# Kernel tuning notes

Measured on AMD Instinct MI355X. Metric: run time of the kernel, lower is better.

The kernel has to match this reference:

```python
import jax, jax.numpy as jnp
import numpy as np

NB_CLASSES = 10  # matches init_kwargs nb_classes


def setup_inputs() -> dict:
    key = jax.random.key(0)
    k1, k2 = jax.random.split(key)
    N, D = 500_000, 64
    h = jax.random.normal(k1, (N, D), dtype=jnp.float32)
    yhat = jax.random.randint(k2, (N,), 0, NB_CLASSES, dtype=jnp.int32)
    return {"h": h, "yhat": yhat}


def reference(h, yhat):
    # Original torch loop: for each class k, gather h_k = h[yhat==k],
    # M_k = mean_i(h_i h_i^T) * 0.5 + I, loss += 0.5 * logdet(M_k).
    # mean of outer products == (masked h)^T @ h / count_k, so we avoid
    # the ragged gather and any [N, D, D] intermediate entirely.
    N, D = h.shape
    eye = jnp.eye(D, dtype=h.dtype)

    def class_term(k):
        mask = (yhat == k).astype(h.dtype)            # [N]
        count = jnp.sum(mask)                         # B_k
        gram = jnp.einsum('nd,ne->de', mask[:, None] * h, h)  # sum_i h_i h_i^T
        M = gram * (0.5 / count) + eye                # [D, D], SPD
        _, logabsdet = jnp.linalg.slogdet(M)
        return 0.5 * logabsdet

    # NB_CLASSES is a small fixed constant -> Python loop is fine & keeps
    # peak memory at one extra [N, D] buffer.
    return jnp.sum(jnp.stack([class_term(k) for k in range(NB_CLASSES)]))
```

## Files before the change

### kernel.cpp

```cpp
#include <hip/hip_runtime.h>
#include <hip/hip_bf16.h>

typedef __attribute__((ext_vector_type(8))) short  short8;
typedef __attribute__((ext_vector_type(4))) float  f32x4;

#define NCLS 10
#define TILE 128
#define TPB  1024
#define NQ   10
#define PPB  (NCLS * NQ * 256)
#define CH   8

#define AS1 __attribute__((address_space(1)))
#define AS3 __attribute__((address_space(3)))

static __device__ inline unsigned short f2bf(float x) {
    unsigned u = __builtin_bit_cast(unsigned, x);
    unsigned r = (u + 0x7FFFu + ((u >> 16) & 1u)) >> 16;
    return (unsigned short)r;
}

static __device__ __forceinline__ void issue_tile(
        const float* __restrict__ h, const int* __restrict__ yhat,
        float* fsb, int* yb, long t, int wid, int lane) {
    const size_t tb = (size_t)t * (TILE * 64);
#pragma unroll
    for (int i = 0; i < 2; ++i) {
        const int C   = (wid * 2 + i) * 64 + lane;
        const int row = C >> 4;
        const int qc  = C & 15;
        const float* gp = h + tb + row * 64 + ((qc ^ (row & 3)) << 2);
        __builtin_amdgcn_global_load_lds((const AS1 float*)gp,
                                         (AS3 float*)(fsb + (wid * 2 + i) * 256),
                                         16, 0, 0);
    }
    if (wid == 0 && lane < 32) {
        const int* gy = yhat + (size_t)t * TILE + lane * 4;
        __builtin_amdgcn_global_load_lds((const AS1 int*)gy, (AS3 int*)yb, 16, 0, 0);
    }
}

template<int NS>
static __device__ __forceinline__ void compute_range(
        const char* hsb, const char* mkb,
        int cls, int ks0, int hi, int col, f32x4 (&acc)[NQ]) {
    const int cb = col << 8;
    const int c7 = col & 7;
#pragma unroll
    for (int s = 0; s < NS; ++s) {
        const int ks = ks0 + s;
        const short8 m = *reinterpret_cast<const short8*>(mkb + cls * 256 + ks * 64 + hi * 16);
        const int x = ((ks * 4 + hi) ^ c7) << 4;
        short8 am[4];
#pragma unroll
        for (int nb = 0; nb < 4; ++nb) {
            short8 r = *reinterpret_cast<const short8*>(hsb + nb * 4096 + cb + x);
            am[nb] = r & m;
        }
        acc[0] = __builtin_amdgcn_mfma_f32_16x16x32_bf16(am[0], am[0], acc[0], 0, 0, 0);
        acc[1] = __builtin_amdgcn_mfma_f32_16x16x32_bf16(am[0], am[1], acc[1], 0, 0, 0);
        acc[2] = __builtin_amdgcn_mfma_f32_16x16x32_bf16(am[0], am[2], acc[2], 0, 0, 0);
        acc[3] = __builtin_amdgcn_mfma_f32_16x16x32_bf16(am[0], am[3], acc[3], 0, 0, 0);
        acc[4] = __builtin_amdgcn_mfma_f32_16x16x32_bf16(am[1], am[1], acc[4], 0, 0, 0);
        acc[5] = __builtin_amdgcn_mfma_f32_16x16x32_bf16(am[1], am[2], acc[5], 0, 0, 0);
        acc[6] = __builtin_amdgcn_mfma_f32_16x16x32_bf16(am[1], am[3], acc[6], 0, 0, 0);
        acc[7] = __builtin_amdgcn_mfma_f32_16x16x32_bf16(am[2], am[2], acc[7], 0, 0, 0);
        acc[8] = __builtin_amdgcn_mfma_f32_16x16x32_bf16(am[2], am[3], acc[8], 0, 0, 0);
        acc[9] = __builtin_amdgcn_mfma_f32_16x16x32_bf16(am[3], am[3], acc[9], 0, 0, 0);
    }
}

__global__ __launch_bounds__(TPB, 4) void HL_gram(
        const float* __restrict__ h, const int* __restrict__ yhat,
        float* __restrict__ partials, int* __restrict__ cntp,
        int N, int ntiles, int G) {
    __shared__ __align__(16) float          fs[2][TILE * 64];
    __shared__ __align__(16) unsigned short hs[2][64 * TILE];
    __shared__ __align__(16) unsigned short mk[2][NCLS * TILE];
    __shared__ __align__(16) int            ylds[2][TILE];
    __shared__ int cntlds[16];

    const int tid  = threadIdx.x;
    const int wid  = tid >> 6;
    const int lane = tid & 63;
    const int hi   = lane >> 4;
    const int col  = lane & 15;
    const int r2   = tid >> 4;
    const int q16  = tid & 15;

    if (tid < 16) cntlds[tid] = 0;

    int cls, ks0, ns;
    if      (wid < 6)  { cls = wid;      ks0 = 0; ns = 2; }
    else if (wid < 10) { cls = wid;      ks0 = 0; ns = 4; }
    else               { cls = wid - 10; ks0 = 2; ns = 2; }

    f32x4 acc[NQ];
#pragma unroll
    for (int q = 0; q < NQ; ++q) acc[q] = (f32x4){0.f, 0.f, 0.f, 0.f};

    const int  bid     = blockIdx.x;
    const int  K       = (ntiles - bid + G - 1) / G;
    const bool partial = (N % TILE) != 0;

    if (!(partial && bid == ntiles - 1))
        issue_tile(h, yhat, &fs[0][0], &ylds[0][0], bid, wid, lane);

    int cur = 0;
    for (int k = 0; k < K; ++k) {
        const long t    = bid + (long)k * G;
        const bool tail = partial && (t == (long)(ntiles - 1));

        __syncthreads();

        f32x4 v[2];
#pragma unroll
        for (int j = 0; j < 2; ++j) {
            const int row = r2 * 2 + j;
            if (!tail) {
                v[j] = *reinterpret_cast<const f32x4*>(
                    (const char*)&fs[cur][0] + ((row * 256 + (q16 << 4)) ^ ((row & 3) << 4)));
            } else {
                const long g = t * TILE + row;
                if (g < N) v[j] = *reinterpret_cast<const f32x4*>(h + (size_t)g * 64 + (q16 << 2));
                else       v[j] = (f32x4){0.f, 0.f, 0.f, 0.f};
            }
        }
#pragma unroll
        for (int q = 0; q < 4; ++q) {
            const int d = q16 * 4 + q;
            unsigned pk = (unsigned)f2bf(v[0][q]) | ((unsigned)f2bf(v[1][q]) << 16);
            *reinterpret_cast<unsigned*>(
                (char*)&hs[cur][0] + ((d * 256 + r2 * 4) ^ ((d & 7) << 4))) = pk;
        }
        if (tid < TILE) {
            int y;
            if (!tail) y = ylds[cur][tid];
            else { const long g = t * TILE + tid; y = (g < N) ? yhat[g] : -1; }
#pragma unroll
            for (int c = 0; c < NCLS; ++c) {
                mk[cur][c * TILE + tid] = (y == c) ? (unsigned short)0xFFFFu : (unsigned short)0u;
                unsigned long long b = __ballot(y == c);
                if (lane == 0) atomicAdd(&cntlds[c], __popcll(b));
            }
        }

        __syncthreads();

        if (k + 1 < K) {
            const long tn = bid + (long)(k + 1) * G;
            if (!(partial && tn == (long)(ntiles - 1)))
                issue_tile(h, yhat, &fs[cur ^ 1][0], &ylds[cur ^ 1][0], tn, wid, lane);
        }

        if (ns == 4) compute_range<4>((const char*)&hs[cur][0], (const char*)&mk[cur][0],
                                      cls, 0,   hi, col, acc);
        else         compute_range<2>((const char*)&hs[cur][0], (const char*)&mk[cur][0],
                                      cls, ks0, hi, col, acc);
        cur ^= 1;
    }

    float* xch = (float*)&fs[0][0];
#pragma unroll
    for (int qq = 0; qq < NQ; qq += 2) {
        __syncthreads();
        if (wid >= 10) {
            float* dst = xch + (wid - 10) * 512;
            *reinterpret_cast<f32x4*>(dst + (lane << 2))       = acc[qq];
            *reinterpret_cast<f32x4*>(dst + 256 + (lane << 2)) = acc[qq + 1];
        }
        __syncthreads();
        if (wid < 6) {
            const float* src = xch + wid * 512;
            acc[qq]     += *reinterpret_cast<const f32x4*>(src + (lane << 2));
            acc[qq + 1] += *reinterpret_cast<const f32x4*>(src + 256 + (lane << 2));
        }
    }

    if (wid < NCLS) {
        float* pb = partials + (size_t)bid * PPB + (size_t)wid * (NQ * 256);
#pragma unroll
        for (int q = 0; q < NQ; ++q)
            *reinterpret_cast<f32x4*>(pb + q * 256 + (lane << 2)) = acc[q];
    }
    if (tid < NCLS) cntp[bid * 16 + tid] = cntlds[tid];
}

__global__ void HL_reduce(const float* __restrict__ partials, float* __restrict__ rpart,
                          float* __restrict__ out, int G, int CS) {
    const int idx = blockIdx.x * blockDim.x + threadIdx.x;
    if (blockIdx.x == 0 && threadIdx.x == 0) out[0] = 0.f;
    if (idx >= CH * NCLS * NQ * 64) return;
    const int ch = idx / (NCLS * NQ * 64);
    const int r  = idx % (NCLS * NQ * 64);
    const int cq = r >> 6;
    const int l  = r & 63;

    int b0 = ch * CS;
    int b1 = b0 + CS; if (b1 > G) b1 = G;

    f32x4 s = (f32x4){0.f, 0.f, 0.f, 0.f};
    const float* p = partials + (size_t)cq * 256 + (l << 2);
    for (int b = b0; b < b1; ++b)
        s += *reinterpret_cast<const f32x4*>(p + (size_t)b * PPB);

    *reinterpret_cast<f32x4*>(rpart + ((size_t)ch * (NCLS * NQ) + cq) * 256 + (l << 2)) = s;
}

__global__ __launch_bounds__(64, 1) void HL_chol(
        const float* __restrict__ rpart, const int* __restrict__ cntp,
        float* __restrict__ out, int G) {
    __shared__ float M[64][68];
    __shared__ float lcol[64];
    const int cls = blockIdx.x;
    const int i   = threadIdx.x;

    int c = 0;
    for (int b = i; b < G; b += 64) c += cntp[b * 16 + cls];
#pragma unroll
    for (int off = 32; off > 0; off >>= 1) c += __shfl_xor(c, off);
    const float inv = 0.5f / (float)c;

    const int QMB[NQ] = {0,0,0,0,1,1,1,2,2,3};
    const int QNB[NQ] = {0,1,2,3,1,2,3,2,3,3};
    const float* rp = rpart + (size_t)cls * (NQ * 256);
#pragma unroll
    for (int q = 0; q < NQ; ++q) {
        f32x4 s = (f32x4){0.f, 0.f, 0.f, 0.f};
#pragma unroll
        for (int ch = 0; ch < CH; ++ch)
            s += *reinterpret_cast<const f32x4*>(rp + (size_t)ch * (NCLS * NQ * 256) + q * 256 + (i << 2));
        const int row0 = QMB[q] * 16 + ((i >> 4) << 2);
        const int colo = QNB[q] * 16 + (i & 15);
#pragma unroll
        for (int rr = 0; rr < 4; ++rr) {
            M[row0 + rr][colo] = s[rr];
            M[colo][row0 + rr] = s[rr];
        }
    }
    __syncthreads();

    float row[64];
#pragma unroll
    for (int c2 = 0; c2 < 64; ++c2)
        row[c2] = M[i][c2] * inv + (c2 == i ? 1.0f : 0.0f);

#pragma unroll
    for (int j = 0; j < 64; ++j) {
        const float piv = __shfl(row[j], j);
        const float li  = row[j] * rsqrtf(piv);
        lcol[i] = li;
        __syncthreads();
#pragma unroll
        for (int c2 = j + 1; c2 < 64; ++c2)
            row[c2] -= li * lcol[c2];
        __syncthreads();
    }

    float slog = 0.f;
#pragma unroll
    for (int j = 0; j < 64; ++j)
        if (i == j) slog = __logf(row[j]);
    slog += __shfl_down(slog, 32); slog += __shfl_down(slog, 16);
    slog += __shfl_down(slog, 8);  slog += __shfl_down(slog, 4);
    slog += __shfl_down(slog, 2);  slog += __shfl_down(slog, 1);
    if (i == 0) atomicAdd(out, 0.5f * slog);
}

extern "C" void kernel_launch(void* const* d_in, const int* in_sizes, int n_in,
                              void* d_out, int out_size, void* d_ws, size_t ws_size,
                              hipStream_t stream) {
    const float* h    = (const float*)d_in[0];
    const int*   yhat = (const int*)d_in[1];
    const int    N    = in_sizes[1];
    float* out = (float*)d_out;

    const size_t rpart_sz = (size_t)CH * NCLS * NQ * 256 * sizeof(float);
    const size_t cntp_off = rpart_sz;

    const int ntiles = (N + TILE - 1) / TILE;
    int G = 256;
    {
        const size_t perG = 64 + (size_t)PPB * sizeof(float);
        if (ws_size > rpart_sz) {
            size_t maxG = (ws_size - rpart_sz) / perG;
            if ((size_t)G > maxG) G = (int)maxG;
        } else G = 1;
        if (G < 1) G = 1;
    }
    if (G > ntiles) G = ntiles;

    const size_t partials_off = cntp_off + (size_t)G * 16 * sizeof(int);
    float* rpart    = (float*)d_ws;
    int*   cntp     = (int*)((char*)d_ws + cntp_off);
    float* partials = (float*)((char*)d_ws + partials_off);

    HL_gram<<<G, TPB, 0, stream>>>(h, yhat, partials, cntp, N, ntiles, G);

    int CS = (G + CH - 1) / CH;
    const int rthreads = CH * NCLS * NQ * 64;
    HL_reduce<<<(rthreads + 255) / 256, 256, 0, stream>>>(partials, rpart, out, G, CS);

    HL_chol<<<NCLS, 64, 0, stream>>>(rpart, cntp, out, G);
}
```

Before: 81.32 us.

## Triple-buffer async tile loads with counted vmcnt waits and clamped tail loads

Deepens the global-to-LDS prefetch from two to three stages, using explicit s_waitcnt vmcnt counts and raw s_barrier in place of __syncthreads, so more loads are in flight while the MFMA stage runs. The tail path now clamps row indices instead of using a separate direct-load branch, and masks out-of-range labels. The fp32-to-bf16 transpose is rewritten so each thread reads 8 scalars and does one 16-byte LDS write with a new XOR swizzle. The reduction chunk count CH also doubles. The extra stage uses more LDS per block, which may lower occupancy, and hand-written waitcnt values are fragile.

```diff
diff --git a/kernel.cpp b/kernel.cpp
--- a/kernel.cpp
+++ b/kernel.cpp
@@ -9,34 +9,36 @@
 #define TPB  1024
 #define NQ   10
 #define PPB  (NCLS * NQ * 256)
-#define CH   8
+#define CH   16
 
 #define AS1 __attribute__((address_space(1)))
 #define AS3 __attribute__((address_space(3)))
 
 static __device__ inline unsigned short f2bf(float x) {
     unsigned u = __builtin_bit_cast(unsigned, x);
-    unsigned r = (u + 0x7FFFu + ((u >> 16) & 1u)) >> 16;
-    return (unsigned short)r;
+    return (unsigned short)((u + 0x7FFFu + ((u >> 16) & 1u)) >> 16);
 }
 
 static __device__ __forceinline__ void issue_tile(
         const float* __restrict__ h, const int* __restrict__ yhat,
-        float* fsb, int* yb, long t, int wid, int lane) {
-    const size_t tb = (size_t)t * (TILE * 64);
+        float* fsb, int* yb, long t, long N, int wid, int lane) {
 #pragma unroll
     for (int i = 0; i < 2; ++i) {
-        const int C   = (wid * 2 + i) * 64 + lane;
-        const int row = C >> 4;
-        const int qc  = C & 15;
-        const float* gp = h + tb + row * 64 + ((qc ^ (row & 3)) << 2);
+        const int C  = wid * 128 + i * 64 + lane;
+        const int n  = C >> 4;
+        const int cc = C & 15;
+        long row = t * TILE + n;
+        if (row > N - 1) row = N - 1;
+        const float* gp = h + row * 64 + ((cc << 2) ^ ((n & 7) << 3));
         __builtin_amdgcn_global_load_lds((const AS1 float*)gp,
                                          (AS3 float*)(fsb + (wid * 2 + i) * 256),
                                          16, 0, 0);
     }
     if (wid == 0 && lane < 32) {
-        const int* gy = yhat + (size_t)t * TILE + lane * 4;
-        __builtin_amdgcn_global_load_lds((const AS1 int*)gy, (AS3 int*)yb, 16, 0, 0);
+        long y0 = t * TILE + lane * 4;
+        if (y0 > N - 4) y0 = N - 4;
+        __builtin_amdgcn_global_load_lds((const AS1 int*)(yhat + y0),
+                                         (AS3 int*)yb, 16, 0, 0);
     }
 }
 
@@ -73,11 +75,11 @@
 __global__ __launch_bounds__(TPB, 4) void HL_gram(
         const float* __restrict__ h, const int* __restrict__ yhat,
         float* __restrict__ partials, int* __restrict__ cntp,
-        int N, int ntiles, int G) {
-    __shared__ __align__(16) float          fs[2][TILE * 64];
+        long N, int ntiles, int G) {
+    __shared__ __align__(16) float          fs[3][TILE * 64];
     __shared__ __align__(16) unsigned short hs[2][64 * TILE];
     __shared__ __align__(16) unsigned short mk[2][NCLS * TILE];
-    __shared__ __align__(16) int            ylds[2][TILE];
+    __shared__ __align__(16) int            ylds[3][TILE];
     __shared__ int cntlds[16];
 
     const int tid  = threadIdx.x;
@@ -85,10 +87,9 @@
     const int lane = tid & 63;
     const int hi   = lane >> 4;
     const int col  = lane & 15;
-    const int r2   = tid >> 4;
-    const int q16  = tid & 15;
 
     if (tid < 16) cntlds[tid] = 0;
+    asm volatile("s_waitcnt lgkmcnt(0)" ::: "memory");
 
     int cls, ks0, ns;
     if      (wid < 6)  { cls = wid;      ks0 = 0; ns = 2; }
@@ -99,65 +100,63 @@
 #pragma unroll
     for (int q = 0; q < NQ; ++q) acc[q] = (f32x4){0.f, 0.f, 0.f, 0.f};
 
-    const int  bid     = blockIdx.x;
-    const int  K       = (ntiles - bid + G - 1) / G;
-    const bool partial = (N % TILE) != 0;
-
-    if (!(partial && bid == ntiles - 1))
-        issue_tile(h, yhat, &fs[0][0], &ylds[0][0], bid, wid, lane);
-
-    int cur = 0;
+    const int bid = blockIdx.x;
+    const int K   = (ntiles - bid + G - 1) / G;
+
+#pragma unroll
+    for (int kk = 0; kk < 3; ++kk)
+        if (kk < K)
+            issue_tile(h, yhat, &fs[kk][0], &ylds[kk][0], bid + (long)kk * G, N, wid, lane);
+
     for (int k = 0; k < K; ++k) {
-        const long t    = bid + (long)k * G;
-        const bool tail = partial && (t == (long)(ntiles - 1));
-
-        __syncthreads();
-
-        f32x4 v[2];
-#pragma unroll
-        for (int j = 0; j < 2; ++j) {
-            const int row = r2 * 2 + j;
-            if (!tail) {
-                v[j] = *reinterpret_cast<const f32x4*>(
-                    (const char*)&fs[cur][0] + ((row * 256 + (q16 << 4)) ^ ((row & 3) << 4)));
-            } else {
-                const long g = t * TILE + row;
-                if (g < N) v[j] = *reinterpret_cast<const f32x4*>(h + (size_t)g * 64 + (q16 << 2));
-                else       v[j] = (f32x4){0.f, 0.f, 0.f, 0.f};
+        const long t  = bid + (long)k * G;
+        const int  bk = k % 3;
+        const int  hk = k & 1;
+        const int  r  = (K - 1 - k) > 2 ? 2 : (K - 1 - k);
+
+        if (wid == 0) {
+            if (r == 2)      asm volatile("s_waitcnt vmcnt(6)" ::: "memory");
+            else if (r == 1) asm volatile("s_waitcnt vmcnt(3)" ::: "memory");
+            else             asm volatile("s_waitcnt vmcnt(0)" ::: "memory");
+        } else {
+            if (r == 2)      asm volatile("s_waitcnt vmcnt(4)" ::: "memory");
+            else if (r == 1) asm volatile("s_waitcnt vmcnt(2)" ::: "memory");
+            else             asm volatile("s_waitcnt vmcnt(0)" ::: "memory");
+        }
+        __builtin_amdgcn_s_barrier();
+
+        {
+            const float* fsb = &fs[bk][0];
+            short8 w;
+#pragma unroll
+            for (int j = 0; j < 8; ++j) {
+                const float x = fsb[(wid * 8 + j) * 64 + (lane ^ (j << 3))];
+                w[j] = (short)f2bf(x);
             }
-        }
-#pragma unroll
-        for (int q = 0; q < 4; ++q) {
-            const int d = q16 * 4 + q;
-            unsigned pk = (unsigned)f2bf(v[0][q]) | ((unsigned)f2bf(v[1][q]) << 16);
-            *reinterpret_cast<unsigned*>(
-                (char*)&hs[cur][0] + ((d * 256 + r2 * 4) ^ ((d & 7) << 4))) = pk;
+            *reinterpret_cast<short8*>(
+                (char*)&hs[hk][0] + lane * 256 + ((wid ^ (lane & 7)) << 4)) = w;
         }
         if (tid < TILE) {
-            int y;
-            if (!tail) y = ylds[cur][tid];
-            else { const long g = t * TILE + tid; y = (g < N) ? yhat[g] : -1; }
+            int y = ylds[bk][tid];
+            if (t * TILE + tid >= N) y = -1;
 #pragma unroll
             for (int c = 0; c < NCLS; ++c) {
-                mk[cur][c * TILE + tid] = (y == c) ? (unsigned short)0xFFFFu : (unsigned short)0u;
+                mk[hk][c * TILE + tid] = (y == c) ? (unsigned short)0xFFFFu : (unsigned short)0u;
                 unsigned long long b = __ballot(y == c);
                 if (lane == 0) atomicAdd(&cntlds[c], __popcll(b));
             }
         }
 
-        __syncthreads();
-
-        if (k + 1 < K) {
-            const long tn = bid + (long)(k + 1) * G;
-            if (!(partial && tn == (long)(ntiles - 1)))
-                issue_tile(h, yhat, &fs[cur ^ 1][0], &ylds[cur ^ 1][0], tn, wid, lane);
-        }
-
-        if (ns == 4) compute_range<4>((const char*)&hs[cur][0], (const char*)&mk[cur][0],
+        asm volatile("s_waitcnt lgkmcnt(0)" ::: "memory");
+        __builtin_amdgcn_s_barrier();
+
+        if (k + 3 < K)
+            issue_tile(h, yhat, &fs[bk][0], &ylds[bk][0], bid + (long)(k + 3) * G, N, wid, lane);
+
+        if (ns == 4) compute_range<4>((const char*)&hs[hk][0], (const char*)&mk[hk][0],
                                       cls, 0,   hi, col, acc);
-        else         compute_range<2>((const char*)&hs[cur][0], (const char*)&mk[cur][0],
+        else         compute_range<2>((const char*)&hs[hk][0], (const char*)&mk[hk][0],
                                       cls, ks0, hi, col, acc);
-        cur ^= 1;
     }
 
     float* xch = (float*)&fs[0][0];
@@ -272,13 +271,13 @@
                               hipStream_t stream) {
     const float* h    = (const float*)d_in[0];
     const int*   yhat = (const int*)d_in[1];
-    const int    N    = in_sizes[1];
+    const long   N    = in_sizes[1];
     float* out = (float*)d_out;
 
     const size_t rpart_sz = (size_t)CH * NCLS * NQ * 256 * sizeof(float);
     const size_t cntp_off = rpart_sz;
 
-    const int ntiles = (N + TILE - 1) / TILE;
+    const int ntiles = (int)((N + TILE - 1) / TILE);
     int G = 256;
     {
         const size_t perG = 64 + (size_t)PPB * sizeof(float);
```

After: 83.79 us. 3.0% more time.
